# Kernel tuning notes

Hardware: AMD Instinct MI355X
Metric: run time of the kernel (lower is better)

The kernel has to match this reference:

```python
import jax, jax.numpy as jnp
import numpy as np

N_NODES = 50000
N_EDGES = 800000
D_IN = 128
D_H = 128
D_OUT = 1
N_GRAPHS = 64
BN_EPS = 1e-5


def _lin(key, i, o):
    return jax.random.normal(key, (i, o), jnp.float32) / np.float32(np.sqrt(i))


def setup_inputs() -> dict:
    key = jax.random.key(0)
    ks = jax.random.split(key, 40)
    inp = {}
    inp["x"] = jax.random.normal(ks[0], (N_NODES, D_IN), jnp.float32)
    inp["edge_index"] = jax.random.randint(ks[1], (2, N_EDGES), 0, N_NODES)
    inp["batch"] = jnp.sort(jax.random.randint(ks[2], (N_NODES,), 0, N_GRAPHS))
    dims = [D_IN, D_H, D_H]
    ki = 3
    for l in range(3):
        inp[f"l{l}_W1"] = _lin(ks[ki], dims[l], D_H); ki += 1
        inp[f"l{l}_b1"] = jnp.zeros((D_H,), jnp.float32)
        inp[f"l{l}_W2"] = _lin(ks[ki], D_H, D_H); ki += 1
        inp[f"l{l}_b2"] = jnp.zeros((D_H,), jnp.float32)
        inp[f"l{l}_g"] = jnp.ones((D_H,), jnp.float32)
        inp[f"l{l}_beta"] = jnp.zeros((D_H,), jnp.float32)
    inp["p_W1"] = _lin(ks[ki], D_H * 3, D_H); ki += 1
    inp["p_b1"] = jnp.zeros((D_H,), jnp.float32)
    inp["p_g"] = jnp.ones((D_H,), jnp.float32)
    inp["p_beta"] = jnp.zeros((D_H,), jnp.float32)
    inp["p_W2"] = _lin(ks[ki], D_H, D_OUT); ki += 1
    inp["p_b2"] = jnp.zeros((D_OUT,), jnp.float32)
    return inp


def _bn(h, g, b):
    # training-mode BatchNorm1d: biased batch statistics over dim 0
    m = h.mean(0)
    v = h.var(0)
    return (h - m) * (g / jnp.sqrt(v + BN_EPS)) + b


def _gin_conv(x, src, dst, W1, b1, W2, b2):
    # scatter-add neighbor aggregation: messages x[src] summed into dst
    agg = jax.ops.segment_sum(x[src], dst, num_segments=N_NODES)
    h = x + agg  # eps = 0 (GINConv default)
    h = jax.nn.relu(h @ W1 + b1)
    return h @ W2 + b2


def reference(x, edge_index, batch,
              l0_W1, l0_b1, l0_W2, l0_b2, l0_g, l0_beta,
              l1_W1, l1_b1, l1_W2, l1_b2, l1_g, l1_beta,
              l2_W1, l2_b1, l2_W2, l2_b2, l2_g, l2_beta,
              p_W1, p_b1, p_g, p_beta, p_W2, p_b2):
    src, dst = edge_index[0], edge_index[1]
    layers = [
        (l0_W1, l0_b1, l0_W2, l0_b2, l0_g, l0_beta),
        (l1_W1, l1_b1, l1_W2, l1_b2, l1_g, l1_beta),
        (l2_W1, l2_b1, l2_W2, l2_b2, l2_g, l2_beta),
    ]
    h = x
    h_list = []
    for (W1, b1, W2, b2, g, beta) in layers:
        h = _gin_conv(h, src, dst, W1, b1, W2, b2)
        h = jax.nn.relu(_bn(h, g, beta))
        # dropout: identity in eval mode
        h_list.append(h)
    # global mean pool per layer, then concat
    cnt = jax.ops.segment_sum(jnp.ones((N_NODES,), jnp.float32), batch,
                              num_segments=N_GRAPHS)
    cnt = jnp.maximum(cnt, 1.0)[:, None]
    pooled = [jax.ops.segment_sum(hh, batch, num_segments=N_GRAPHS) / cnt
              for hh in h_list]
    z = jnp.concatenate(pooled, axis=1)  # [G, 3*D_H]
    # prediction MLP: fc1 -> relu -> bn -> fc2 (dropout identity)
    z = jax.nn.relu(z @ p_W1 + p_b1)
    z = _bn(z, p_g, p_beta)
    return z @ p_W2 + p_b2  # [G, D_OUT]
```

## Files before the change

kernel.cpp:

```cpp
#include <hip/hip_runtime.h>

#define NN 50000
#define NE 800000
#define D  128
#define NG 64
#define BN_EPS 1e-5f
#define SCAN_B 196

typedef __attribute__((ext_vector_type(8))) short short8;
typedef __attribute__((ext_vector_type(4))) float f32x4;

static __device__ inline unsigned short f2bf_rn(float f) {
  unsigned u = __float_as_uint(f);
  unsigned r = (u + 0x7FFF + ((u >> 16) & 1)) >> 16;
  return (unsigned short)r;
}
static __device__ inline float bf2f(unsigned short h) {
  return __uint_as_float((unsigned)h << 16);
}

__global__ void k_hist(const int* __restrict__ dst, int* __restrict__ counts) {
  int e = blockIdx.x * blockDim.x + threadIdx.x;
  if (e < NE) atomicAdd(&counts[dst[e]], 1);
}

__global__ void k_scan1(const int* __restrict__ counts, int* __restrict__ bsum) {
  const int t = threadIdx.x;
  const int i = blockIdx.x * 256 + t;
  int v = (i < NN) ? counts[i] : 0;
  #pragma unroll
  for (int d = 32; d >= 1; d >>= 1) v += __shfl_xor(v, d, 64);
  __shared__ int ws[4];
  if ((t & 63) == 0) ws[t >> 6] = v;
  __syncthreads();
  if (t == 0) bsum[blockIdx.x] = ws[0] + ws[1] + ws[2] + ws[3];
}

__global__ void k_scan2(const int* __restrict__ bsum, int* __restrict__ boff,
                        int* __restrict__ offs) {
  const int t = threadIdx.x, lane = t & 63, w = t >> 6;
  int v = (t < SCAN_B) ? bsum[t] : 0;
  int s = v;
  #pragma unroll
  for (int d = 1; d < 64; d <<= 1) { int u = __shfl_up(s, d, 64); if (lane >= d) s += u; }
  __shared__ int ws[4];
  if (lane == 63) ws[w] = s;
  __syncthreads();
  int add = 0;
  for (int k = 0; k < w; ++k) add += ws[k];
  if (t < SCAN_B) boff[t] = add + s - v;
  if (t == SCAN_B - 1) offs[NN] = add + s;
}

__global__ void k_scan3(const int* __restrict__ counts, const int* __restrict__ boff,
                        int* __restrict__ offs) {
  const int t = threadIdx.x, lane = t & 63, w = t >> 6;
  const int i = blockIdx.x * 256 + t;
  int v = (i < NN) ? counts[i] : 0;
  int s = v;
  #pragma unroll
  for (int d = 1; d < 64; d <<= 1) { int u = __shfl_up(s, d, 64); if (lane >= d) s += u; }
  __shared__ int ws[4];
  if (lane == 63) ws[w] = s;
  __syncthreads();
  int add = 0;
  for (int k = 0; k < w; ++k) add += ws[k];
  if (i < NN) offs[i] = boff[blockIdx.x] + add + s - v;
}

__global__ void k_scatter(const int* __restrict__ src, const int* __restrict__ dst,
                          const int* __restrict__ offs, int* __restrict__ cursor,
                          int* __restrict__ esrc) {
  int e = blockIdx.x * blockDim.x + threadIdx.x;
  if (e < NE) {
    int d = dst[e];
    int p = offs[d] + atomicAdd(&cursor[d], 1);
    esrc[p] = src[e];
  }
}

__global__ void k_gbounds(const int* __restrict__ batch, int* __restrict__ gstart) {
  const int g = threadIdx.x;
  if (g > NG) return;
  int lo = 0, hi = NN;
  while (lo < hi) { int mid = (lo + hi) >> 1; if (batch[mid] < g) lo = mid + 1; else hi = mid; }
  gstart[g] = lo;
}

__global__ __launch_bounds__(256) void k_cvt(const float* __restrict__ X,
                                             unsigned long long* __restrict__ Xb) {
  const int n4 = NN * D / 4;
  for (int i = blockIdx.x * blockDim.x + threadIdx.x; i < n4; i += gridDim.x * blockDim.x) {
    float4 v = ((const float4*)X)[i];
    unsigned long long p = (unsigned long long)f2bf_rn(v.x) |
                           ((unsigned long long)f2bf_rn(v.y) << 16) |
                           ((unsigned long long)f2bf_rn(v.z) << 32) |
                           ((unsigned long long)f2bf_rn(v.w) << 48);
    Xb[i] = p;
  }
}

struct WPtrs { const float* w[6]; };
__global__ void k_prep6(WPtrs ws, short* __restrict__ wb) {
  const int widx = blockIdx.y;
  const float* __restrict__ W = ws.w[widx];
  short* __restrict__ Wh = wb + (size_t)(widx * 2) * 16384;
  short* __restrict__ Wl = Wh + 16384;
  const int idx = blockIdx.x * 256 + threadIdx.x;
  const int k = idx >> 7, c = idx & 127;
  const float v = W[idx];
  const unsigned short h = f2bf_rn(v);
  const unsigned short lo = f2bf_rn(v - bf2f(h));
  const int o = ((k >> 5) * 128 + c) * 32 + (k & 31);
  Wh[o] = (short)h;
  Wl[o] = (short)lo;
}

template<bool BN>
__global__ __launch_bounds__(256) void k_aggregate(const unsigned* __restrict__ Hb,
                                                   const int* __restrict__ offs,
                                                   const int* __restrict__ esrc,
                                                   const float* __restrict__ sums,
                                                   const float* __restrict__ sumsq,
                                                   const float* __restrict__ gw,
                                                   const float* __restrict__ beta,
                                                   float* __restrict__ zstats,
                                                   unsigned* __restrict__ AGGh,
                                                   unsigned* __restrict__ AGGl) {
  if (blockIdx.x == 0 && threadIdx.x < 256) zstats[threadIdx.x] = 0.f;

  const int node = blockIdx.x * 4 + (threadIdx.x >> 6);
  const int lane = threadIdx.x & 63;
  float2 sc = make_float2(1.f, 1.f), sh = make_float2(0.f, 0.f);
  if (BN) {
    const float2 s2 = ((const float2*)sums)[lane];
    const float2 q2 = ((const float2*)sumsq)[lane];
    const float2 g2 = ((const float2*)gw)[lane];
    const float2 b2 = ((const float2*)beta)[lane];
    const float mx = s2.x * (1.f / NN), my = s2.y * (1.f / NN);
    sc.x = g2.x / sqrtf(q2.x * (1.f / NN) - mx * mx + BN_EPS);
    sc.y = g2.y / sqrtf(q2.y * (1.f / NN) - my * my + BN_EPS);
    sh.x = b2.x - mx * sc.x;
    sh.y = b2.y - my * sc.y;
  }

  auto rd = [&](int r) -> float2 {
    const unsigned u = Hb[r * 64 + lane];
    float2 v = make_float2(bf2f((unsigned short)u), bf2f((unsigned short)(u >> 16)));
    if (BN) {
      v.x = fmaxf(fmaf(v.x, sc.x, sh.x), 0.f);
      v.y = fmaxf(fmaf(v.y, sc.y, sh.y), 0.f);
    }
    return v;
  };

  float2 acc = rd(node);
  const int b = offs[node], e = offs[node + 1];
  int i = b;
  for (; i + 8 <= e; i += 8) {
    const int s0 = esrc[i],     s1 = esrc[i + 1], s2 = esrc[i + 2], s3 = esrc[i + 3];
    const int s4 = esrc[i + 4], s5 = esrc[i + 5], s6 = esrc[i + 6], s7 = esrc[i + 7];
    const float2 v0 = rd(s0), v1 = rd(s1), v2 = rd(s2), v3 = rd(s3);
    const float2 v4 = rd(s4), v5 = rd(s5), v6 = rd(s6), v7 = rd(s7);
    acc.x += ((v0.x + v1.x) + (v2.x + v3.x)) + ((v4.x + v5.x) + (v6.x + v7.x));
    acc.y += ((v0.y + v1.y) + (v2.y + v3.y)) + ((v4.y + v5.y) + (v6.y + v7.y));
  }
  for (; i + 4 <= e; i += 4) {
    const int s0 = esrc[i], s1 = esrc[i + 1], s2 = esrc[i + 2], s3 = esrc[i + 3];
    const float2 v0 = rd(s0), v1 = rd(s1), v2 = rd(s2), v3 = rd(s3);
    acc.x += (v0.x + v1.x) + (v2.x + v3.x);
    acc.y += (v0.y + v1.y) + (v2.y + v3.y);
  }
  for (; i < e; ++i) {
    const float2 v = rd(esrc[i]);
    acc.x += v.x; acc.y += v.y;
  }
  const unsigned short hx = f2bf_rn(acc.x), hy = f2bf_rn(acc.y);
  AGGh[node * 64 + lane] = (unsigned)hx | ((unsigned)hy << 16);
  const unsigned short lx = f2bf_rn(acc.x - bf2f(hx)), ly = f2bf_rn(acc.y - bf2f(hy));
  AGGl[node * 64 + lane] = (unsigned)lx | ((unsigned)ly << 16);
}

__global__ __launch_bounds__(512) void k_mlp2(const short* __restrict__ Ah,
                                              const short* __restrict__ Al,
                                              const short* __restrict__ W1h, const short* __restrict__ W1l,
                                              const short* __restrict__ W2h, const short* __restrict__ W2l,
                                              const float* __restrict__ b1, const float* __restrict__ b2,
                                              short* __restrict__ Hb,
                                              float* __restrict__ stats) {
  __shared__ __align__(16) short regA[32768];
  __shared__ __align__(16) short regB[32768];

  const int t = threadIdx.x;
  {
    const short8* __restrict__ g1h = (const short8*)W1h;
    const short8* __restrict__ g1l = (const short8*)W1l;
    const short8* __restrict__ g2h = (const short8*)W2h;
    const short8* __restrict__ g2l = (const short8*)W2l;
    short8* a8 = (short8*)regA;
    short8* b8 = (short8*)regB;
    #pragma unroll
    for (int i = 0; i < 4; ++i) {
      a8[i * 512 + t]        = g1h[i * 512 + t];
      a8[2048 + i * 512 + t] = g1l[i * 512 + t];
      b8[i * 512 + t]        = g2h[i * 512 + t];
      b8[2048 + i * 512 + t] = g2l[i * 512 + t];
    }
  }

  const int l = t & 63, w = t >> 6;
  const int lr = l & 15, fq = l >> 4, lk = fq * 8;
  const int rg = w & 3;
  const int cg = w >> 2;
  const int row0 = blockIdx.x * 128;

  short8 ah[2][4], al[2][4];
  {
    const short8 z = (short8)(0);
    #pragma unroll
    for (int rt = 0; rt < 2; ++rt) {
      const int arow = row0 + rg * 32 + rt * 16 + lr;
      const bool ok = arow < NN;
      #pragma unroll
      for (int kc = 0; kc < 4; ++kc) {
        ah[rt][kc] = ok ? *(const short8*)(Ah + (size_t)arow * D + kc * 32 + lk) : z;
        al[rt][kc] = ok ? *(const short8*)(Al + (size_t)arow * D + kc * 32 + lk) : z;
      }
    }
  }
  __syncthreads();

  f32x4 acc[2][4];
  #pragma unroll
  for (int rt = 0; rt < 2; ++rt)
    #pragma unroll
    for (int ct = 0; ct < 4; ++ct) acc[rt][ct] = (f32x4)(0.f);
  #pragma unroll
  for (int kc = 0; kc < 4; ++kc) {
    #pragma unroll
    for (int ct = 0; ct < 4; ++ct) {
      const int wc = cg * 64 + ct * 16 + lr;
      const short8 bh = *(const short8*)(&regA[(kc * 128 + wc) * 32 + lk]);
      const short8 bl = *(const short8*)(&regA[16384 + (kc * 128 + wc) * 32 + lk]);
      #pragma unroll
      for (int rt = 0; rt < 2; ++rt) {
        acc[rt][ct] = __builtin_amdgcn_mfma_f32_16x16x32_bf16(ah[rt][kc], bh, acc[rt][ct], 0, 0, 0);
        acc[rt][ct] = __builtin_amdgcn_mfma_f32_16x16x32_bf16(al[rt][kc], bh, acc[rt][ct], 0, 0, 0);
        acc[rt][ct] = __builtin_amdgcn_mfma_f32_16x16x32_bf16(ah[rt][kc], bl, acc[rt][ct], 0, 0, 0);
      }
    }
  }
  __syncthreads();

  #pragma unroll
  for (int rt = 0; rt < 2; ++rt) {
    #pragma unroll
    for (int ct = 0; ct < 4; ++ct) {
      const int c = cg * 64 + ct * 16 + lr;
      const float bb = b1[c];
      #pragma unroll
      for (int j = 0; j < 4; ++j) {
        const int r = rg * 32 + rt * 16 + fq * 4 + j;
        const int swc = c ^ ((r & 7) << 3);
        const float v = fmaxf(acc[rt][ct][j] + bb, 0.f);
        const unsigned short h = f2bf_rn(v);
        regA[r * 128 + swc] = (short)h;
        regA[16384 + r * 128 + swc] = (short)f2bf_rn(v - bf2f(h));
      }
    }
  }
  __syncthreads();

  f32x4 acc2[2][4];
  #pragma unroll
  for (int rt = 0; rt < 2; ++rt)
    #pragma unroll
    for (int ct = 0; ct < 4; ++ct) acc2[rt][ct] = (f32x4)(0.f);
  #pragma unroll
  for (int kc = 0; kc < 4; ++kc) {
    short8 ch[2], cl[2];
    #pragma unroll
    for (int rt = 0; rt < 2; ++rt) {
      const int r = rg * 32 + rt * 16 + lr;
      const int swb = r * 128 + ((kc * 32 + lk) ^ ((r & 7) << 3));
      ch[rt] = *(const short8*)(regA + swb);
      cl[rt] = *(const short8*)(regA + 16384 + swb);
    }
    #pragma unroll
    for (int ct = 0; ct < 4; ++ct) {
      const int wc = cg * 64 + ct * 16 + lr;
      const short8 bh = *(const short8*)(&regB[(kc * 128 + wc) * 32 + lk]);
      const short8 bl = *(const short8*)(&regB[16384 + (kc * 128 + wc) * 32 + lk]);
      #pragma unroll
      for (int rt = 0; rt < 2; ++rt) {
        acc2[rt][ct] = __builtin_amdgcn_mfma_f32_16x16x32_bf16(ch[rt], bh, acc2[rt][ct], 0, 0, 0);
        acc2[rt][ct] = __builtin_amdgcn_mfma_f32_16x16x32_bf16(cl[rt], bh, acc2[rt][ct], 0, 0, 0);
        acc2[rt][ct] = __builtin_amdgcn_mfma_f32_16x16x32_bf16(ch[rt], bl, acc2[rt][ct], 0, 0, 0);
      }
    }
  }

  float ps[4], pq[4];
  #pragma unroll
  for (int ct = 0; ct < 4; ++ct) { ps[ct] = 0.f; pq[ct] = 0.f; }
  #pragma unroll
  for (int rt = 0; rt < 2; ++rt) {
    #pragma unroll
    for (int ct = 0; ct < 4; ++ct) {
      const int c = cg * 64 + ct * 16 + lr;
      const float bb = b2[c];
      #pragma unroll
      for (int j = 0; j < 4; ++j) {
        const int gr = row0 + rg * 32 + rt * 16 + fq * 4 + j;
        if (gr < NN) {
          const float v = acc2[rt][ct][j] + bb;
          Hb[(size_t)gr * D + c] = (short)f2bf_rn(v);
          ps[ct] += v; pq[ct] += v * v;
        }
      }
    }
  }
  __syncthreads();
  float* red  = (float*)regA;
  float* redq = red + 16 * 132;
  const int grp = rg * 4 + fq;
  #pragma unroll
  for (int ct = 0; ct < 4; ++ct) {
    const int c = cg * 64 + ct * 16 + lr;
    red [grp * 132 + c] = ps[ct];
    redq[grp * 132 + c] = pq[ct];
  }
  __syncthreads();
  if (t < 128) {
    float s = 0.f, q = 0.f;
    #pragma unroll
    for (int g2 = 0; g2 < 16; ++g2) { s += red[g2 * 132 + t]; q += redq[g2 * 132 + t]; }
    atomicAdd(&stats[t], s);
    atomicAdd(&stats[128 + t], q);
  }
}

__global__ __launch_bounds__(256) void k_pool(const unsigned short* __restrict__ Hb,
                                              const float* __restrict__ sums,
                                              const float* __restrict__ sumsq,
                                              const float* __restrict__ gw,
                                              const float* __restrict__ beta,
                                              const int* __restrict__ gstart,
                                              float* __restrict__ pooled, int lofs) {
  const int g = blockIdx.y;
  const int s = gstart[g], e = gstart[g + 1];
  const int t = threadIdx.x, c = t & 127, half = t >> 7;
  const float m  = sums[c] * (1.f / NN);
  const float sc = gw[c] / sqrtf(sumsq[c] * (1.f / NN) - m * m + BN_EPS);
  const float sh = beta[c] - m * sc;
  const int len = e - s;
  const int nchunk = (int)gridDim.x;
  const int per = (len + nchunk - 1) / nchunk;
  const int r0 = s + (int)blockIdx.x * per;
  const int r1 = min(e, r0 + per);
  float sum = 0.f;
  for (int r = r0 + half; r < r1; r += 2)
    sum += fmaxf(fmaf(bf2f(Hb[r * D + c]), sc, sh), 0.f);
  __shared__ float red[256];
  red[t] = sum;
  __syncthreads();
  if (t < 128) atomicAdd(&pooled[g * 384 + lofs + c], red[t] + red[t + 128]);
}

__global__ __launch_bounds__(128) void k_fc1(const float* __restrict__ pooled,
                                             const int* __restrict__ gstart,
                                             const float* __restrict__ W1,
                                             const float* __restrict__ b1,
                                             float* __restrict__ z1) {
  const int g = blockIdx.x, j = threadIdx.x;
  __shared__ float p[384];
  const float cnt = (float)(gstart[g + 1] - gstart[g]);
  const float inv = 1.f / fmaxf(cnt, 1.f);
  for (int k = j; k < 384; k += 128) p[k] = pooled[g * 384 + k] * inv;
  __syncthreads();
  float acc = b1[j];
  #pragma unroll 8
  for (int k = 0; k < 384; ++k) acc = fmaf(p[k], W1[k * 128 + j], acc);
  z1[g * 128 + j] = fmaxf(acc, 0.f);
}

__global__ __launch_bounds__(128) void k_head(const float* __restrict__ z1,
                                              const float* __restrict__ g,
                                              const float* __restrict__ beta,
                                              const float* __restrict__ W2,
                                              const float* __restrict__ b2,
                                              float* __restrict__ out) {
  __shared__ float z2[NG][129];
  __shared__ float w2s[128];
  const int j = threadIdx.x;
  w2s[j] = W2[j];
  float vals[NG];
  float s = 0.f, q = 0.f;
  for (int gg = 0; gg < NG; ++gg) {
    float v = z1[gg * 128 + j];
    vals[gg] = v; s += v; q += v * v;
  }
  const float m   = s / (float)NG;
  const float var = q / (float)NG - m * m;
  const float sc  = g[j] / sqrtf(var + BN_EPS);
  const float sh  = beta[j] - m * sc;
  for (int gg = 0; gg < NG; ++gg) z2[gg][j] = vals[gg] * sc + sh;
  __syncthreads();
  if (j < NG) {
    float acc = b2[0];
    #pragma unroll 8
    for (int k = 0; k < 128; ++k) acc += z2[j][k] * w2s[k];
    out[j] = acc;
  }
}

extern "C" void kernel_launch(void* const* d_in, const int* in_sizes, int n_in,
                              void* d_out, int out_size, void* d_ws, size_t ws_size,
                              hipStream_t stream) {
  const float* x     = (const float*)d_in[0];
  const int*   e_src = (const int*)d_in[1];
  const int*   e_dst = e_src + NE;
  const int*   batch = (const int*)d_in[2];
  const float *lW1[3], *lb1[3], *lW2[3], *lb2[3], *lg[3], *lbeta[3];
  for (int l = 0; l < 3; ++l) {
    lW1[l]   = (const float*)d_in[3 + 6 * l + 0];
    lb1[l]   = (const float*)d_in[3 + 6 * l + 1];
    lW2[l]   = (const float*)d_in[3 + 6 * l + 2];
    lb2[l]   = (const float*)d_in[3 + 6 * l + 3];
    lg[l]    = (const float*)d_in[3 + 6 * l + 4];
    lbeta[l] = (const float*)d_in[3 + 6 * l + 5];
  }
  const float* pW1   = (const float*)d_in[21];
  const float* pb1   = (const float*)d_in[22];
  const float* pg    = (const float*)d_in[23];
  const float* pbeta = (const float*)d_in[24];
  const float* pW2   = (const float*)d_in[25];
  const float* pb2   = (const float*)d_in[26];
  float* out = (float*)d_out;

  char* w = (char*)d_ws;
  auto alloc = [&](size_t bytes) { char* p = w; w += (bytes + 255) & ~(size_t)255; return p; };
  short* AGGh   = (short*)alloc((size_t)NN * D * 2);
  short* AGGl   = (short*)alloc((size_t)NN * D * 2);
  short* Hb0    = (short*)alloc((size_t)NN * D * 2);
  short* Hb1    = (short*)alloc((size_t)NN * D * 2);
  short* xb     = Hb1;
  int*   counts = (int*)alloc((size_t)NN * 4);
  int*   cursor = (int*)alloc((size_t)NN * 4);
  int*   offs   = (int*)alloc((size_t)(NN + 1) * 4);
  int*   esrc   = (int*)alloc((size_t)NE * 4);
  int*   bsum   = (int*)alloc((size_t)SCAN_B * 4);
  int*   boff   = (int*)alloc((size_t)SCAN_B * 4);
  int*   gstart = (int*)alloc((size_t)(NG + 1) * 4);
  float* stats  = (float*)alloc((size_t)3 * 256 * 4);
  float* pooled = (float*)alloc((size_t)NG * 384 * 4);
  float* z1     = (float*)alloc((size_t)NG * 128 * 4);
  short* wb     = (short*)alloc((size_t)12 * 32768);
  auto st = [&](int l) { return stats + (size_t)l * 256; };

  hipMemsetAsync(counts, 0, (size_t)NN * 4, stream);
  hipMemsetAsync(cursor, 0, (size_t)NN * 4, stream);
  hipMemsetAsync(pooled, 0, (size_t)NG * 384 * 4, stream);

  k_hist   <<<(NE + 255) / 256, 256, 0, stream>>>(e_dst, counts);
  k_scan1  <<<SCAN_B, 256, 0, stream>>>(counts, bsum);
  k_scan2  <<<1, 256, 0, stream>>>(bsum, boff, offs);
  k_scan3  <<<SCAN_B, 256, 0, stream>>>(counts, boff, offs);
  k_scatter<<<(NE + 255) / 256, 256, 0, stream>>>(e_src, e_dst, offs, cursor, esrc);
  k_gbounds<<<1, 128, 0, stream>>>(batch, gstart);
  k_cvt    <<<1024, 256, 0, stream>>>(x, (unsigned long long*)xb);

  WPtrs ws;
  ws.w[0] = lW1[0]; ws.w[1] = lW2[0];
  ws.w[2] = lW1[1]; ws.w[3] = lW2[1];
  ws.w[4] = lW1[2]; ws.w[5] = lW2[2];
  k_prep6<<<dim3(64, 6), 256, 0, stream>>>(ws, wb);
  auto plane = [&](int widx, int hilo) { return wb + (size_t)(widx * 2 + hilo) * 16384; };

  short* Hbuf[2] = {Hb0, Hb1};
  const int mlp_grid = (NN + 127) / 128;
  for (int l = 0; l < 3; ++l) {
    if (l == 0)
      k_aggregate<false><<<NN / 4, 256, 0, stream>>>((const unsigned*)xb, offs, esrc,
                                                     nullptr, nullptr, nullptr, nullptr,
                                                     st(0), (unsigned*)AGGh, (unsigned*)AGGl);
    else
      k_aggregate<true><<<NN / 4, 256, 0, stream>>>((const unsigned*)Hbuf[(l - 1) & 1], offs, esrc,
                                                    st(l - 1), st(l - 1) + 128, lg[l - 1], lbeta[l - 1],
                                                    st(l), (unsigned*)AGGh, (unsigned*)AGGl);
    k_mlp2<<<mlp_grid, 512, 0, stream>>>(AGGh, AGGl,
                                         plane(2 * l, 0), plane(2 * l, 1),
                                         plane(2 * l + 1, 0), plane(2 * l + 1, 1),
                                         lb1[l], lb2[l], Hbuf[l & 1], st(l));
    k_pool <<<dim3(8, NG), 256, 0, stream>>>((const unsigned short*)Hbuf[l & 1],
                                             st(l), st(l) + 128, lg[l], lbeta[l],
                                             gstart, pooled, l * 128);
  }

  k_fc1 <<<NG, 128, 0, stream>>>(pooled, gstart, pW1, pb1, z1);
  k_head<<<1, 128, 0, stream>>>(z1, pg, pbeta, pW2, pb2, out);
}
```

Baseline: 389.0 us.

## Fuse mean-pool into next-layer aggregation and merge graph-bounds into convert kernel

The per-layer pooling of layers 0 and 1 moves into the next layer's aggregation kernel. That kernel already computes each node's BN+ReLU value, so it atomically adds the value into the pooled buffer, and the separate pool launches for those layers are dropped. The graph-boundary binary search is folded into an extra block of the fp32-to-bf16 conversion kernel, and the neighbour gather loop is unrolled to 16 loads. This removes two pool kernels and one small launch, in exchange for heavy global float atomics: 50000 nodes times 128 values contend on only 64 graph rows per layer, which may serialize.

New measurement: 739.2 us. 90.0% more time.

```diff
diff --git a/kernel.cpp b/kernel.cpp
--- a/kernel.cpp
+++ b/kernel.cpp
@@ -79,18 +79,22 @@
   }
 }
 
-__global__ void k_gbounds(const int* __restrict__ batch, int* __restrict__ gstart) {
-  const int g = threadIdx.x;
-  if (g > NG) return;
-  int lo = 0, hi = NN;
-  while (lo < hi) { int mid = (lo + hi) >> 1; if (batch[mid] < g) lo = mid + 1; else hi = mid; }
-  gstart[g] = lo;
-}
-
 __global__ __launch_bounds__(256) void k_cvt(const float* __restrict__ X,
-                                             unsigned long long* __restrict__ Xb) {
+                                             unsigned long long* __restrict__ Xb,
+                                             const int* __restrict__ batch,
+                                             int* __restrict__ gstart) {
+  if (blockIdx.x == gridDim.x - 1) {
+    const int g = threadIdx.x;
+    if (g <= NG) {
+      int lo = 0, hi = NN;
+      while (lo < hi) { int mid = (lo + hi) >> 1; if (batch[mid] < g) lo = mid + 1; else hi = mid; }
+      gstart[g] = lo;
+    }
+    return;
+  }
   const int n4 = NN * D / 4;
-  for (int i = blockIdx.x * blockDim.x + threadIdx.x; i < n4; i += gridDim.x * blockDim.x) {
+  const int nb = gridDim.x - 1;
+  for (int i = blockIdx.x * blockDim.x + threadIdx.x; i < n4; i += nb * blockDim.x) {
     float4 v = ((const float4*)X)[i];
     unsigned long long p = (unsigned long long)f2bf_rn(v.x) |
                            ((unsigned long long)f2bf_rn(v.y) << 16) |
@@ -125,6 +129,8 @@
                                                    const float* __restrict__ gw,
                                                    const float* __restrict__ beta,
                                                    float* __restrict__ zstats,
+                                                   const int* __restrict__ batch,
+                                                   float* __restrict__ pooled, int lofs,
                                                    unsigned* __restrict__ AGGh,
                                                    unsigned* __restrict__ AGGl) {
   if (blockIdx.x == 0 && threadIdx.x < 256) zstats[threadIdx.x] = 0.f;
@@ -155,15 +161,21 @@
   };
 
   float2 acc = rd(node);
+  if (BN) {
+    float* pd = pooled + (size_t)batch[node] * 384 + lofs + lane * 2;
+    atomicAdd(pd, acc.x);
+    atomicAdd(pd + 1, acc.y);
+  }
   const int b = offs[node], e = offs[node + 1];
   int i = b;
-  for (; i + 8 <= e; i += 8) {
-    const int s0 = esrc[i],     s1 = esrc[i + 1], s2 = esrc[i + 2], s3 = esrc[i + 3];
-    const int s4 = esrc[i + 4], s5 = esrc[i + 5], s6 = esrc[i + 6], s7 = esrc[i + 7];
-    const float2 v0 = rd(s0), v1 = rd(s1), v2 = rd(s2), v3 = rd(s3);
-    const float2 v4 = rd(s4), v5 = rd(s5), v6 = rd(s6), v7 = rd(s7);
-    acc.x += ((v0.x + v1.x) + (v2.x + v3.x)) + ((v4.x + v5.x) + (v6.x + v7.x));
-    acc.y += ((v0.y + v1.y) + (v2.y + v3.y)) + ((v4.y + v5.y) + (v6.y + v7.y));
+  for (; i + 16 <= e; i += 16) {
+    float2 v[16];
+    #pragma unroll
+    for (int q = 0; q < 16; ++q) v[q] = rd(esrc[i + q]);
+    float sx = 0.f, sy = 0.f;
+    #pragma unroll
+    for (int q = 0; q < 16; ++q) { sx += v[q].x; sy += v[q].y; }
+    acc.x += sx; acc.y += sy;
   }
   for (; i + 4 <= e; i += 4) {
     const int s0 = esrc[i], s1 = esrc[i + 1], s2 = esrc[i + 2], s3 = esrc[i + 3];
@@ -467,8 +479,7 @@
   k_scan2  <<<1, 256, 0, stream>>>(bsum, boff, offs);
   k_scan3  <<<SCAN_B, 256, 0, stream>>>(counts, boff, offs);
   k_scatter<<<(NE + 255) / 256, 256, 0, stream>>>(e_src, e_dst, offs, cursor, esrc);
-  k_gbounds<<<1, 128, 0, stream>>>(batch, gstart);
-  k_cvt    <<<1024, 256, 0, stream>>>(x, (unsigned long long*)xb);
+  k_cvt    <<<1025, 256, 0, stream>>>(x, (unsigned long long*)xb, batch, gstart);
 
   WPtrs ws;
   ws.w[0] = lW1[0]; ws.w[1] = lW2[0];
@@ -483,19 +494,21 @@
     if (l == 0)
       k_aggregate<false><<<NN / 4, 256, 0, stream>>>((const unsigned*)xb, offs, esrc,
                                                      nullptr, nullptr, nullptr, nullptr,
-                                                     st(0), (unsigned*)AGGh, (unsigned*)AGGl);
+                                                     st(0), batch, nullptr, 0,
+                                                     (unsigned*)AGGh, (unsigned*)AGGl);
     else
       k_aggregate<true><<<NN / 4, 256, 0, stream>>>((const unsigned*)Hbuf[(l - 1) & 1], offs, esrc,
                                                     st(l - 1), st(l - 1) + 128, lg[l - 1], lbeta[l - 1],
-                                                    st(l), (unsigned*)AGGh, (unsigned*)AGGl);
+                                                    st(l), batch, pooled, (l - 1) * 128,
+                                                    (unsigned*)AGGh, (unsigned*)AGGl);
     k_mlp2<<<mlp_grid, 512, 0, stream>>>(AGGh, AGGl,
                                          plane(2 * l, 0), plane(2 * l, 1),
                                          plane(2 * l + 1, 0), plane(2 * l + 1, 1),
                                          lb1[l], lb2[l], Hbuf[l & 1], st(l));
-    k_pool <<<dim3(8, NG), 256, 0, stream>>>((const unsigned short*)Hbuf[l & 1],
-                                             st(l), st(l) + 128, lg[l], lbeta[l],
-                                             gstart, pooled, l * 128);
-  }
+  }
+  k_pool<<<dim3(8, NG), 256, 0, stream>>>((const unsigned short*)Hbuf[2 & 1],
+                                          st(2), st(2) + 128, lg[2], lbeta[2],
+                                          gstart, pooled, 2 * 128);
 
   k_fc1 <<<NG, 128, 0, stream>>>(pooled, gstart, pW1, pb1, z1);
   k_head<<<1, 128, 0, stream>>>(z1, pg, pbeta, pW2, pb2, out);
```
